# Performance work log

Measured on AMD Instinct MI355X. Metric: run time of the kernel, lower is better.

## Reference

```python
import jax, jax.numpy as jnp
import numpy as np

B, S, D = 4, 2048, 1024
H, DK = 16, 64
NEG = -1e9


def setup_inputs() -> dict:
    key = jax.random.key(0)
    ks = jax.random.split(key, 6)
    hidden_states = jax.random.normal(ks[0], (B, S, D), dtype=jnp.float32)
    # evidence-constrained mask: causal mask plus random evidence restriction
    causal = jnp.tril(jnp.ones((S, S), dtype=bool))
    evid = jax.random.bernoulli(ks[1], 0.7, (S, S))
    allowed = causal & (evid | jnp.eye(S, dtype=bool))  # diag always allowed
    attention_mask = jnp.where(allowed, 0.0, NEG).astype(jnp.float32)
    scale = 0.02
    Wq = jax.random.normal(ks[2], (H * DK, D), dtype=jnp.float32) * scale
    Wk = jax.random.normal(ks[3], (H * DK, D), dtype=jnp.float32) * scale
    Wv = jax.random.normal(ks[4], (H * DK, D), dtype=jnp.float32) * scale
    Wo = jax.random.normal(ks[5], (D, H * DK), dtype=jnp.float32) * scale
    return {"hidden_states": hidden_states, "attention_mask": attention_mask,
            "Wq": Wq, "Wk": Wk, "Wv": Wv, "Wo": Wo}


def reference(hidden_states, attention_mask, Wq, Wk, Wv, Wo):
    b, s, _ = hidden_states.shape
    # nn.Linear(bias=False): y = x @ W.T ; reshape to (B,H,S,DK)
    def proj(x, W):
        y = jnp.einsum('bsd,ed->bse', x, W)
        return y.reshape(b, s, H, DK).transpose(0, 2, 1, 3)
    q = proj(hidden_states, Wq)
    k = proj(hidden_states, Wk)
    v = proj(hidden_states, Wv)
    logits = jnp.einsum('bhqd,bhkd->bhqk', q, k) / jnp.sqrt(jnp.float32(DK))
    logits = logits + attention_mask[None, None, :, :]
    attn = jax.nn.softmax(logits, axis=-1)
    ctx = jnp.einsum('bhqk,bhkd->bhqd', attn, v)
    ctx = ctx.transpose(0, 2, 1, 3).reshape(b, s, H * DK)
    out = jnp.einsum('bse,de->bsd', ctx, Wo)
    return out
```

## Files before the change

### kernel.cpp

```cpp
#include <hip/hip_runtime.h>
#include <hip/hip_bf16.h>
#include <math.h>

#define B_  4
#define S_  2048
#define D_  1024
#define H_  16
#define DK_ 64
#define M_  (B_*S_)
#define E_  (H_*DK_)
#define LOG2E  1.4426950408889634f
#define QSCALE 0.18033688011112042f

typedef short  bf16x8 __attribute__((ext_vector_type(8)));
typedef float  f32x4  __attribute__((ext_vector_type(4)));
typedef unsigned short u16;

__device__ __forceinline__ u16 f2b(float x) {
    __hip_bfloat16 h = __float2bfloat16(x);
    return *(u16*)&h;
}

__device__ __forceinline__ void async16(const u16* g, u16* l) {
    __builtin_amdgcn_global_load_lds(
        (const __attribute__((address_space(1))) unsigned int*)g,
        (__attribute__((address_space(3))) unsigned int*)l, 16, 0, 0);
}

__global__ __launch_bounds__(256)
void cvt_x(const float* __restrict__ s, u16* __restrict__ d, int n8) {
    int i = blockIdx.x * 256 + threadIdx.x;
    if (i >= n8) return;
    const float4* s4 = (const float4*)s;
    float4 a = s4[2 * i], b = s4[2 * i + 1];
    u16 o[8] = {f2b(a.x), f2b(a.y), f2b(a.z), f2b(a.w),
                f2b(b.x), f2b(b.y), f2b(b.z), f2b(b.w)};
    *(uint4*)(d + (size_t)8 * i) = *(const uint4*)o;
}

__global__ __launch_bounds__(256)
void cvt_w4(const float* __restrict__ s0, const float* __restrict__ s1,
            const float* __restrict__ s2, const float* __restrict__ s3,
            u16* __restrict__ d0, u16* __restrict__ d1,
            u16* __restrict__ d2, u16* __restrict__ d3, int n8) {
    const float* s = blockIdx.y == 0 ? s0 : blockIdx.y == 1 ? s1 : blockIdx.y == 2 ? s2 : s3;
    u16*         d = blockIdx.y == 0 ? d0 : blockIdx.y == 1 ? d1 : blockIdx.y == 2 ? d2 : d3;
    int i = blockIdx.x * 256 + threadIdx.x;
    if (i >= n8) return;
    const float4* s4 = (const float4*)s;
    float4 a = s4[2 * i], b = s4[2 * i + 1];
    u16 o[8] = {f2b(a.x), f2b(a.y), f2b(a.z), f2b(a.w),
                f2b(b.x), f2b(b.y), f2b(b.z), f2b(b.w)};
    *(uint4*)(d + (size_t)8 * i) = *(const uint4*)o;
}

__device__ __forceinline__ void gemm_core(
    const u16* __restrict__ Ag, const u16* __restrict__ Bg, int K,
    int bm, int bn, u16* As, u16* Bs, f32x4 (&acc)[4][4])
{
    const int tid  = threadIdx.x;
    const int w    = tid >> 6, lane = tid & 63;
    const int l15  = lane & 15, quad = lane >> 4;
    const int wm   = (w >> 1) * 64, wn = (w & 1) * 64;
    const int srow = lane >> 3;
    const int sg   = (lane & 7) ^ srow;
    const int sx   = l15 & 7;

    for (int k0 = 0; k0 < K; k0 += 64) {
        __syncthreads();
        #pragma unroll
        for (int i = 0; i < 4; i++) {
            const int row = w * 32 + i * 8 + srow;
            async16(Ag + (size_t)(bm + row) * K + k0 + sg * 8,
                    As + (size_t)(w * 32 + i * 8) * 64);
            async16(Bg + (size_t)(bn + row) * K + k0 + sg * 8,
                    Bs + (size_t)(w * 32 + i * 8) * 64);
        }
        __syncthreads();

        #pragma unroll
        for (int s = 0; s < 2; s++) {
            bf16x8 af[4], bf[4];
            #pragma unroll
            for (int i = 0; i < 4; i++)
                af[i] = *(const bf16x8*)(As + (size_t)(wm + i * 16 + l15) * 64
                                            + (((s * 4 + quad) ^ sx) * 8));
            #pragma unroll
            for (int j = 0; j < 4; j++)
                bf[j] = *(const bf16x8*)(Bs + (size_t)(wn + j * 16 + l15) * 64
                                            + (((s * 4 + quad) ^ sx) * 8));
            #pragma unroll
            for (int i = 0; i < 4; i++)
                #pragma unroll
                for (int j = 0; j < 4; j++)
                    acc[i][j] = __builtin_amdgcn_mfma_f32_16x16x32_bf16(af[i], bf[j], acc[i][j], 0, 0, 0);
        }
    }
}

__global__ __launch_bounds__(256)
void gemm_qkv(const u16* __restrict__ Xb,
              const u16* __restrict__ Wqb, const u16* __restrict__ Wkb,
              const u16* __restrict__ Wvb,
              u16* __restrict__ Qm, u16* __restrict__ Km, u16* __restrict__ Vt)
{
    __shared__ u16 As[128 * 64];
    __shared__ u16 Bs[128 * 64];
    const int bm    = blockIdx.x * 128;
    const int nb    = blockIdx.y;
    const int which = nb >> 3;
    const int col0  = (nb & 7) * 128;
    const u16* Bg = which == 0 ? Wqb : which == 1 ? Wkb : Wvb;

    f32x4 acc[4][4] = {};
    gemm_core(Xb, Bg, D_, bm, col0, As, Bs, acc);

    const int tid = threadIdx.x;
    const int w   = tid >> 6, lane = tid & 63;
    const int l15 = lane & 15, quad = lane >> 4;
    const int wm  = (w >> 1) * 64, wn = (w & 1) * 64;

    if (which == 2) {
        #pragma unroll
        for (int i = 0; i < 4; i++)
            #pragma unroll
            for (int j = 0; j < 4; j++) {
                int c    = col0 + wn + j * 16 + l15;
                int tok0 = bm + wm + i * 16 + quad * 4;
                u16 pk[4] = {f2b(acc[i][j][0]), f2b(acc[i][j][1]),
                             f2b(acc[i][j][2]), f2b(acc[i][j][3])};
                size_t idx = (((size_t)((tok0 >> 11) * E_ + c)) << 11) + (tok0 & 2047);
                *(uint2*)(Vt + idx) = *(const uint2*)pk;
            }
    } else {
        u16* Cm = which == 0 ? Qm : Km;
        const float sc = which == 0 ? QSCALE : 1.0f;
        #pragma unroll
        for (int i = 0; i < 4; i++)
            #pragma unroll
            for (int j = 0; j < 4; j++)
                #pragma unroll
                for (int r = 0; r < 4; r++) {
                    int row = bm + wm + i * 16 + quad * 4 + r;
                    int c   = col0 + wn + j * 16 + l15;
                    Cm[(size_t)row * E_ + c] = f2b(acc[i][j][r] * sc);
                }
    }
}

__global__ __launch_bounds__(256)
void gemm_out(const u16* __restrict__ Cmx, const u16* __restrict__ Wob,
              float* __restrict__ out)
{
    __shared__ u16 As[128 * 64];
    __shared__ u16 Bs[128 * 64];
    const int bm = blockIdx.x * 128;
    const int bn = blockIdx.y * 128;

    f32x4 acc[4][4] = {};
    gemm_core(Cmx, Wob, E_, bm, bn, As, Bs, acc);

    const int tid = threadIdx.x;
    const int w   = tid >> 6, lane = tid & 63;
    const int l15 = lane & 15, quad = lane >> 4;
    const int wm  = (w >> 1) * 64, wn = (w & 1) * 64;
    #pragma unroll
    for (int i = 0; i < 4; i++)
        #pragma unroll
        for (int j = 0; j < 4; j++)
            #pragma unroll
            for (int r = 0; r < 4; r++)
                out[(size_t)(bm + wm + i * 16 + quad * 4 + r) * D_ + bn + wn + j * 16 + l15]
                    = acc[i][j][r];
}

__global__ __launch_bounds__(256)
void flash_attn(const u16* __restrict__ Q, const u16* __restrict__ Kc,
                const u16* __restrict__ Vt, const float* __restrict__ mask,
                u16* __restrict__ ctx)
{
    const int bh  = blockIdx.x;
    const int qt  = (gridDim.y - 1) - blockIdx.y;
    const int b   = bh >> 4, h = bh & 15;
    const int tid = threadIdx.x;
    const int w   = tid >> 6, lane = tid & 63;
    const int l15 = lane & 15, quad = lane >> 4;
    const int q0  = qt * 128;
    const int nkt = 2 * qt + 2;

    __shared__ u16 Ks[2][64 * 64];
    __shared__ u16 Vs[2][64 * 64];
    __shared__ u16 Ps[4][2][16 * 64];

    bf16x8 qf[2][2];
    #pragma unroll
    for (int s = 0; s < 2; s++) {
        const u16* qb = Q + ((size_t)(b * S_ + q0 + w * 32 + s * 16 + l15)) * E_ + h * DK_;
        qf[s][0] = *(const bf16x8*)(qb + quad * 8);
        qf[s][1] = *(const bf16x8*)(qb + 32 + quad * 8);
    }

    f32x4 acc[2][4] = {};
    float lsum[2] = {0.f, 0.f};

    const int sr = lane >> 3;
    const int sg = (lane & 7) ^ sr;
    const int sx = l15 & 7;

    #pragma unroll
    for (int i = 0; i < 2; i++) {
        const int row8 = w * 16 + i * 8;
        async16(Kc + ((size_t)(b * S_ + row8 + sr)) * E_ + h * DK_ + sg * 8,
                &Ks[0][row8 * 64]);
        async16(Vt + ((size_t)(bh * DK_ + row8 + sr)) * S_ + sg * 8,
                &Vs[0][row8 * 64]);
    }

    for (int kt = 0; kt < nkt; ++kt) {
        const int k0  = kt * 64;
        const int buf = kt & 1;
        __syncthreads();

        f32x4 st[2][4] = {};
        #pragma unroll
        for (int t = 0; t < 4; t++) {
            bf16x8 kf0 = *(const bf16x8*)(&Ks[buf][(t * 16 + l15) * 64 + ((quad ^ sx) * 8)]);
            bf16x8 kf1 = *(const bf16x8*)(&Ks[buf][(t * 16 + l15) * 64 + (((4 + quad) ^ sx) * 8)]);
            st[0][t] = __builtin_amdgcn_mfma_f32_16x16x32_bf16(kf0, qf[0][0], st[0][t], 0, 0, 0);
            st[0][t] = __builtin_amdgcn_mfma_f32_16x16x32_bf16(kf1, qf[0][1], st[0][t], 0, 0, 0);
            st[1][t] = __builtin_amdgcn_mfma_f32_16x16x32_bf16(kf0, qf[1][0], st[1][t], 0, 0, 0);
            st[1][t] = __builtin_amdgcn_mfma_f32_16x16x32_bf16(kf1, qf[1][1], st[1][t], 0, 0, 0);
        }

        if (kt + 1 < nkt) {
            const int k1 = k0 + 64, nb = buf ^ 1;
            #pragma unroll
            for (int i = 0; i < 2; i++) {
                const int row8 = w * 16 + i * 8;
                async16(Kc + ((size_t)(b * S_ + k1 + row8 + sr)) * E_ + h * DK_ + sg * 8,
                        &Ks[nb][row8 * 64]);
                async16(Vt + ((size_t)(bh * DK_ + row8 + sr)) * S_ + k1 + sg * 8,
                        &Vs[nb][row8 * 64]);
            }
        }

        #pragma unroll
        for (int s = 0; s < 2; s++) {
            const float* mp = mask + (size_t)(q0 + w * 32 + s * 16 + l15) * S_ + k0 + quad * 4;
            float4 mk[4];
            #pragma unroll
            for (int t = 0; t < 4; t++) mk[t] = *(const float4*)(mp + t * 16);
            u16* Pw = &Ps[w][s][0];
            float ls = 0.f;
            #pragma unroll
            for (int t = 0; t < 4; t++) {
                float p0 = exp2f(fmaf(mk[t].x, LOG2E, st[s][t][0]));
                float p1 = exp2f(fmaf(mk[t].y, LOG2E, st[s][t][1]));
                float p2 = exp2f(fmaf(mk[t].z, LOG2E, st[s][t][2]));
                float p3 = exp2f(fmaf(mk[t].w, LOG2E, st[s][t][3]));
                ls += (p0 + p1) + (p2 + p3);
                u16 pk[4] = {f2b(p0), f2b(p1), f2b(p2), f2b(p3)};
                *(uint2*)(Pw + l15 * 64 + (((2 * t + (quad >> 1)) ^ sx) * 8) + (quad & 1) * 4)
                    = *(const uint2*)pk;
            }
            lsum[s] += ls;
        }

        #pragma unroll
        for (int sb = 0; sb < 2; sb++) {
            bf16x8 pf0 = *(const bf16x8*)(&Ps[w][0][l15 * 64 + (((4 * sb + quad) ^ sx) * 8)]);
            bf16x8 pf1 = *(const bf16x8*)(&Ps[w][1][l15 * 64 + (((4 * sb + quad) ^ sx) * 8)]);
            #pragma unroll
            for (int nt = 0; nt < 4; nt++) {
                bf16x8 vf = *(const bf16x8*)(&Vs[buf][(nt * 16 + l15) * 64 + (((4 * sb + quad) ^ sx) * 8)]);
                acc[0][nt] = __builtin_amdgcn_mfma_f32_16x16x32_bf16(pf0, vf, acc[0][nt], 0, 0, 0);
                acc[1][nt] = __builtin_amdgcn_mfma_f32_16x16x32_bf16(pf1, vf, acc[1][nt], 0, 0, 0);
            }
        }
    }

    #pragma unroll
    for (int s = 0; s < 2; s++) {
        float ls = lsum[s];
        ls += __shfl_xor(ls, 16, 64);
        ls += __shfl_xor(ls, 32, 64);
        float linv = 1.0f / ls;
        float ir[4];
        #pragma unroll
        for (int r = 0; r < 4; r++) ir[r] = __shfl(linv, quad * 4 + r, 16);
        #pragma unroll
        for (int r = 0; r < 4; r++) {
            size_t orow = ((size_t)(b * S_ + q0 + w * 32 + s * 16 + quad * 4 + r)) * E_ + h * DK_;
            #pragma unroll
            for (int nt = 0; nt < 4; nt++)
                ctx[orow + nt * 16 + l15] = f2b(acc[s][nt][r] * ir[r]);
        }
    }
}

extern "C" void kernel_launch(void* const* d_in, const int* in_sizes, int n_in,
                              void* d_out, int out_size, void* d_ws, size_t ws_size,
                              hipStream_t stream) {
    const float* X    = (const float*)d_in[0];
    const float* mask = (const float*)d_in[1];
    const float* Wq   = (const float*)d_in[2];
    const float* Wk   = (const float*)d_in[3];
    const float* Wv   = (const float*)d_in[4];
    const float* Wo   = (const float*)d_in[5];
    float* out = (float*)d_out;

    char* p = (char*)d_ws;
    u16* Qm  = (u16*)p; p += (size_t)M_ * E_ * 2;
    u16* Km  = (u16*)p; p += (size_t)M_ * E_ * 2;
    u16* Vt  = (u16*)p; p += (size_t)M_ * E_ * 2;
    u16* Wqb = (u16*)p; p += (size_t)E_ * D_ * 2;
    u16* Wkb = (u16*)p; p += (size_t)E_ * D_ * 2;
    u16* Wvb = (u16*)p; p += (size_t)E_ * D_ * 2;
    u16* Wob = (u16*)p; p += (size_t)D_ * E_ * 2;
    u16* Xb  = (u16*)p;
    u16* Cm  = Xb;

    cvt_x<<<(M_ * D_ / 8 + 255) / 256, 256, 0, stream>>>(X, Xb, M_ * D_ / 8);
    cvt_w4<<<dim3(E_ * D_ / 8 / 256, 4), 256, 0, stream>>>(Wq, Wk, Wv, Wo,
                                                           Wqb, Wkb, Wvb, Wob, E_ * D_ / 8);

    gemm_qkv<<<dim3(M_ / 128, 24), 256, 0, stream>>>(Xb, Wqb, Wkb, Wvb, Qm, Km, Vt);

    flash_attn<<<dim3(B_ * H_, S_ / 128), 256, 0, stream>>>(Qm, Km, Vt, mask, Cm);

    gemm_out<<<dim3(M_ / 128, D_ / 128), 256, 0, stream>>>(Cm, Wob, out);
}
```

Measured before the change: 306.6 us.

## Single-buffer attention LDS with register prefetch and merge conversion kernels

The flash attention kernel drops its double-buffered async global-to-LDS loads. It now prefetches the next K/V tile into registers and stores them into a single LDS buffer between two barriers. The P staging buffer is cut to one 16x64 tile per wave, reused for each query sub-block, so LDS per block roughly halves. The aim is higher occupancy, at the cost of an extra barrier per iteration and less asynchronous overlap. The two fp32-to-bf16 conversion kernels are also merged into one launch.

```diff
diff --git a/kernel.cpp b/kernel.cpp
--- a/kernel.cpp
+++ b/kernel.cpp
@@ -27,31 +27,29 @@
         (__attribute__((address_space(3))) unsigned int*)l, 16, 0, 0);
 }
 
+#define XN8 (M_ * D_ / 8)
+#define WN8 (E_ * D_ / 8)
 __global__ __launch_bounds__(256)
-void cvt_x(const float* __restrict__ s, u16* __restrict__ d, int n8) {
-    int i = blockIdx.x * 256 + threadIdx.x;
-    if (i >= n8) return;
+void cvt_all(const float* __restrict__ X,
+             const float* __restrict__ Wq, const float* __restrict__ Wk,
+             const float* __restrict__ Wv, const float* __restrict__ Wo,
+             u16* __restrict__ Xb,
+             u16* __restrict__ Wqb, u16* __restrict__ Wkb,
+             u16* __restrict__ Wvb, u16* __restrict__ Wob) {
+    int idx = blockIdx.x * 256 + threadIdx.x;
+    const float* s; u16* d; int off;
+    if (idx < XN8) { s = X; d = Xb; off = idx; }
+    else {
+        int j = idx - XN8;
+        int which = j / WN8; off = j - which * WN8;
+        s = which == 0 ? Wq : which == 1 ? Wk : which == 2 ? Wv : Wo;
+        d = which == 0 ? Wqb : which == 1 ? Wkb : which == 2 ? Wvb : Wob;
+    }
     const float4* s4 = (const float4*)s;
-    float4 a = s4[2 * i], b = s4[2 * i + 1];
+    float4 a = s4[2 * off], b = s4[2 * off + 1];
     u16 o[8] = {f2b(a.x), f2b(a.y), f2b(a.z), f2b(a.w),
                 f2b(b.x), f2b(b.y), f2b(b.z), f2b(b.w)};
-    *(uint4*)(d + (size_t)8 * i) = *(const uint4*)o;
-}
-
-__global__ __launch_bounds__(256)
-void cvt_w4(const float* __restrict__ s0, const float* __restrict__ s1,
-            const float* __restrict__ s2, const float* __restrict__ s3,
-            u16* __restrict__ d0, u16* __restrict__ d1,
-            u16* __restrict__ d2, u16* __restrict__ d3, int n8) {
-    const float* s = blockIdx.y == 0 ? s0 : blockIdx.y == 1 ? s1 : blockIdx.y == 2 ? s2 : s3;
-    u16*         d = blockIdx.y == 0 ? d0 : blockIdx.y == 1 ? d1 : blockIdx.y == 2 ? d2 : d3;
-    int i = blockIdx.x * 256 + threadIdx.x;
-    if (i >= n8) return;
-    const float4* s4 = (const float4*)s;
-    float4 a = s4[2 * i], b = s4[2 * i + 1];
-    u16 o[8] = {f2b(a.x), f2b(a.y), f2b(a.z), f2b(a.w),
-                f2b(b.x), f2b(b.y), f2b(b.z), f2b(b.w)};
-    *(uint4*)(d + (size_t)8 * i) = *(const uint4*)o;
+    *(uint4*)(d + (size_t)8 * off) = *(const uint4*)o;
 }
 
 __device__ __forceinline__ void gemm_core(
@@ -188,9 +186,9 @@
     const int q0  = qt * 128;
     const int nkt = 2 * qt + 2;
 
-    __shared__ u16 Ks[2][64 * 64];
-    __shared__ u16 Vs[2][64 * 64];
-    __shared__ u16 Ps[4][2][16 * 64];
+    __shared__ u16 Ks[64 * 64];
+    __shared__ u16 Vs[64 * 64];
+    __shared__ u16 Ps[4][16 * 64];
 
     bf16x8 qf[2][2];
     #pragma unroll
@@ -207,50 +205,54 @@
     const int sg = (lane & 7) ^ sr;
     const int sx = l15 & 7;
 
+    uint4 kreg[2], vreg[2];
     #pragma unroll
     for (int i = 0; i < 2; i++) {
         const int row8 = w * 16 + i * 8;
-        async16(Kc + ((size_t)(b * S_ + row8 + sr)) * E_ + h * DK_ + sg * 8,
-                &Ks[0][row8 * 64]);
-        async16(Vt + ((size_t)(bh * DK_ + row8 + sr)) * S_ + sg * 8,
-                &Vs[0][row8 * 64]);
+        kreg[i] = *(const uint4*)(Kc + ((size_t)(b * S_ + row8 + sr)) * E_ + h * DK_ + sg * 8);
+        vreg[i] = *(const uint4*)(Vt + ((size_t)(bh * DK_ + row8 + sr)) * S_ + sg * 8);
     }
 
     for (int kt = 0; kt < nkt; ++kt) {
-        const int k0  = kt * 64;
-        const int buf = kt & 1;
+        const int k0 = kt * 64;
+
         __syncthreads();
+        #pragma unroll
+        for (int i = 0; i < 2; i++) {
+            const int row8 = w * 16 + i * 8;
+            *(uint4*)(Ks + row8 * 64 + lane * 8) = kreg[i];
+            *(uint4*)(Vs + row8 * 64 + lane * 8) = vreg[i];
+        }
+        __syncthreads();
+
+        if (kt + 1 < nkt) {
+            const int k1 = k0 + 64;
+            #pragma unroll
+            for (int i = 0; i < 2; i++) {
+                const int row8 = w * 16 + i * 8;
+                kreg[i] = *(const uint4*)(Kc + ((size_t)(b * S_ + k1 + row8 + sr)) * E_ + h * DK_ + sg * 8);
+                vreg[i] = *(const uint4*)(Vt + ((size_t)(bh * DK_ + k1 >= 0 ? (bh * DK_ + row8 + sr) : 0)) * S_ + k1 + sg * 8);
+            }
+        }
 
         f32x4 st[2][4] = {};
         #pragma unroll
         for (int t = 0; t < 4; t++) {
-            bf16x8 kf0 = *(const bf16x8*)(&Ks[buf][(t * 16 + l15) * 64 + ((quad ^ sx) * 8)]);
-            bf16x8 kf1 = *(const bf16x8*)(&Ks[buf][(t * 16 + l15) * 64 + (((4 + quad) ^ sx) * 8)]);
+            bf16x8 kf0 = *(const bf16x8*)(Ks + (t * 16 + l15) * 64 + ((quad ^ sx) * 8));
+            bf16x8 kf1 = *(const bf16x8*)(Ks + (t * 16 + l15) * 64 + (((4 + quad) ^ sx) * 8));
             st[0][t] = __builtin_amdgcn_mfma_f32_16x16x32_bf16(kf0, qf[0][0], st[0][t], 0, 0, 0);
             st[0][t] = __builtin_amdgcn_mfma_f32_16x16x32_bf16(kf1, qf[0][1], st[0][t], 0, 0, 0);
             st[1][t] = __builtin_amdgcn_mfma_f32_16x16x32_bf16(kf0, qf[1][0], st[1][t], 0, 0, 0);
             st[1][t] = __builtin_amdgcn_mfma_f32_16x16x32_bf16(kf1, qf[1][1], st[1][t], 0, 0, 0);
         }
 
-        if (kt + 1 < nkt) {
-            const int k1 = k0 + 64, nb = buf ^ 1;
-            #pragma unroll
-            for (int i = 0; i < 2; i++) {
-                const int row8 = w * 16 + i * 8;
-                async16(Kc + ((size_t)(b * S_ + k1 + row8 + sr)) * E_ + h * DK_ + sg * 8,
-                        &Ks[nb][row8 * 64]);
-                async16(Vt + ((size_t)(bh * DK_ + row8 + sr)) * S_ + k1 + sg * 8,
-                        &Vs[nb][row8 * 64]);
-            }
-        }
-
+        u16* Pw = &Ps[w][0];
         #pragma unroll
         for (int s = 0; s < 2; s++) {
             const float* mp = mask + (size_t)(q0 + w * 32 + s * 16 + l15) * S_ + k0 + quad * 4;
             float4 mk[4];
             #pragma unroll
             for (int t = 0; t < 4; t++) mk[t] = *(const float4*)(mp + t * 16);
-            u16* Pw = &Ps[w][s][0];
             float ls = 0.f;
             #pragma unroll
             for (int t = 0; t < 4; t++) {
@@ -264,17 +266,15 @@
                     = *(const uint2*)pk;
             }
             lsum[s] += ls;
-        }
-
-        #pragma unroll
-        for (int sb = 0; sb < 2; sb++) {
-            bf16x8 pf0 = *(const bf16x8*)(&Ps[w][0][l15 * 64 + (((4 * sb + quad) ^ sx) * 8)]);
-            bf16x8 pf1 = *(const bf16x8*)(&Ps[w][1][l15 * 64 + (((4 * sb + quad) ^ sx) * 8)]);
-            #pragma unroll
-            for (int nt = 0; nt < 4; nt++) {
-                bf16x8 vf = *(const bf16x8*)(&Vs[buf][(nt * 16 + l15) * 64 + (((4 * sb + quad) ^ sx) * 8)]);
-                acc[0][nt] = __builtin_amdgcn_mfma_f32_16x16x32_bf16(pf0, vf, acc[0][nt], 0, 0, 0);
-                acc[1][nt] = __builtin_amdgcn_mfma_f32_16x16x32_bf16(pf1, vf, acc[1][nt], 0, 0, 0);
+
+            #pragma unroll
+            for (int sb = 0; sb < 2; sb++) {
+                bf16x8 pf = *(const bf16x8*)(Pw + l15 * 64 + (((4 * sb + quad) ^ sx) * 8));
+                #pragma unroll
+                for (int nt = 0; nt < 4; nt++) {
+                    bf16x8 vf = *(const bf16x8*)(Vs + (nt * 16 + l15) * 64 + (((4 * sb + quad) ^ sx) * 8));
+                    acc[s][nt] = __builtin_amdgcn_mfma_f32_16x16x32_bf16(pf, vf, acc[s][nt], 0, 0, 0);
+                }
             }
         }
     }
@@ -320,9 +320,8 @@
     u16* Xb  = (u16*)p;
     u16* Cm  = Xb;
 
-    cvt_x<<<(M_ * D_ / 8 + 255) / 256, 256, 0, stream>>>(X, Xb, M_ * D_ / 8);
-    cvt_w4<<<dim3(E_ * D_ / 8 / 256, 4), 256, 0, stream>>>(Wq, Wk, Wv, Wo,
-                                                           Wqb, Wkb, Wvb, Wob, E_ * D_ / 8);
+    cvt_all<<<(XN8 + 4 * WN8 + 255) / 256, 256, 0, stream>>>(
+        X, Wq, Wk, Wv, Wo, Xb, Wqb, Wkb, Wvb, Wob);
 
     gemm_qkv<<<dim3(M_ / 128, 24), 256, 0, stream>>>(Xb, Wqb, Wkb, Wvb, Qm, Km, Vt);
 
```

After: 365.2 us. 1.19x slower.
